# Kernel optimization log

Hardware: AMD Instinct MI355X
Metric: run time of the kernel (lower is better)

Reference implementation:

```python
import jax, jax.numpy as jnp
import numpy as np

N_NODES = 50_000
N_EDGES = 1_600_000
D = 128          # input_dim == hidden_dim
L = 3            # num_layers
NUM_GRAPHS = 64
LN_EPS = 1e-5


def setup_inputs() -> dict:
    key = jax.random.key(0)
    ks = jax.random.split(key, 12)
    x = jax.random.normal(ks[0], (N_NODES, D), dtype=jnp.float32)
    edge_index = jax.random.randint(ks[1], (2, N_EDGES), 0, N_NODES, dtype=jnp.int64)
    edge_weight = jax.random.normal(ks[2], (N_EDGES,), dtype=jnp.float32)  # signed
    batch = jnp.sort(jax.random.randint(ks[3], (N_NODES,), 0, NUM_GRAPHS, dtype=jnp.int64))
    W_pos = jax.random.normal(ks[4], (L, D, D), dtype=jnp.float32) * 0.05
    b_pos = jnp.zeros((L, D), dtype=jnp.float32)
    W_neg = jax.random.normal(ks[5], (L, D, D), dtype=jnp.float32) * 0.05
    b_neg = jnp.zeros((L, D), dtype=jnp.float32)
    ln_gamma = jnp.ones((D,), dtype=jnp.float32)
    ln_beta = jnp.zeros((D,), dtype=jnp.float32)
    return dict(x=x, edge_index=edge_index, edge_weight=edge_weight, batch=batch,
                W_pos=W_pos, b_pos=b_pos, W_neg=W_neg, b_neg=b_neg,
                ln_gamma=ln_gamma, ln_beta=ln_beta)


def gcn_conv(x, src, dst, w, W, b):
    """PyG GCNConv with edge weights: lin -> sym-normalized scatter-add -> +bias.
    Self-loops (weight 1) are handled analytically instead of appending edges.
    Edges with weight 0 contribute nothing (equivalent to sign-masking the edge set)."""
    n = x.shape[0]
    xw = x @ W                                              # [N, D]
    deg = jax.ops.segment_sum(w, dst, num_segments=n) + 1.0  # +1 for self-loop; >= 1
    dinv = jax.lax.rsqrt(deg)                                # deg^{-1/2}
    norm = dinv[src] * w * dinv[dst]                         # [E]
    agg = jax.ops.segment_sum(norm[:, None] * xw[src], dst, num_segments=n)
    agg = agg + (dinv * dinv)[:, None] * xw                  # self-loop message: xw / deg
    return agg + b


def reference(x, edge_index, edge_weight, batch, W_pos, b_pos, W_neg, b_neg, ln_gamma, ln_beta):
    src, dst = edge_index[0], edge_index[1]
    # sign-split as zero-weight edges: identical math to boolean-masked edge subsets
    w_pos = jnp.maximum(edge_weight, 0.0)
    w_neg = jnp.maximum(-edge_weight, 0.0)
    for l in range(L):
        px = gcn_conv(x, src, dst, w_pos, W_pos[l], b_pos[l])
        nx = gcn_conv(x, src, dst, w_neg, W_neg[l], b_neg[l])
        x = jax.nn.relu(px) - jax.nn.relu(nx)
    # global_mean_pool
    sums = jax.ops.segment_sum(x, batch, num_segments=NUM_GRAPHS)
    counts = jax.ops.segment_sum(jnp.ones((x.shape[0],), x.dtype), batch, num_segments=NUM_GRAPHS)
    pooled = sums / jnp.maximum(counts, 1.0)[:, None]        # [G, D]
    # LayerNorm over feature dim
    mu = pooled.mean(-1, keepdims=True)
    var = ((pooled - mu) ** 2).mean(-1, keepdims=True)
    return (pooled - mu) * jax.lax.rsqrt(var + LN_EPS) * ln_gamma + ln_beta
```

## Files before the change

### kernel.cpp

```cpp
#include <hip/hip_runtime.h>
#include <hip/hip_fp16.h>

#define D 128
#define NG 64
#define WPB 4
#define TILE 4096
#define BSH 7
#define BNODES 128
#define CAP 4608
#define MASK40 ((1ULL << 40) - 1)
#define FPSCALE 1048576.0f
#define INV_FPSCALE (1.0f / 1048576.0f)
#define GEMM_GRID 512
typedef unsigned int uint;
typedef unsigned long long u64;
typedef _Float16 f16x8 __attribute__((ext_vector_type(8)));
typedef float f32x4 __attribute__((ext_vector_type(4)));

__global__ void k_prep(const float* __restrict__ x, __half* __restrict__ xo,
                       const float* __restrict__ Wp, const float* __restrict__ Wn,
                       __half* __restrict__ wpt, __half* __restrict__ wnt,
                       float* sums, float* cnt, int* bktcur,
                       int total4, int nbuk) {
    int i = blockIdx.x * blockDim.x + threadIdx.x;
    if (i < total4) {
        float4 f = ((const float4*)x)[i];
        __half2 h0 = __floats2half2_rn(f.x, f.y);
        __half2 h1 = __floats2half2_rn(f.z, f.w);
        uint2 st;
        st.x = *(uint*)&h0; st.y = *(uint*)&h1;
        ((uint2*)xo)[i] = st;
    }
    if (i < 3 * 128 * 128) {
        int l = i >> 14;
        int r = i & 16383;
        int col = r >> 7, k = r & 127;
        size_t src = ((size_t)l << 14) + ((size_t)k << 7) + col;
        wpt[i] = __float2half_rn(Wp[src]);
        wnt[i] = __float2half_rn(Wn[src]);
    }
    if (i < NG * D) sums[i] = 0.0f;
    if (i < NG) cnt[i] = 0.0f;
    if (i < nbuk) bktcur[i] = i * CAP;
}

__global__ __launch_bounds__(256) void k_bucket(const int* __restrict__ ei,
                                                const float* __restrict__ ew,
                                                int* bktcur, uint2* rec,
                                                int E, int nbuk) {
    __shared__ int h2[256];
    __shared__ int lofs[512];
    __shared__ int gbase[512];
    __shared__ int lcur[512];
    __shared__ uint2 stg[TILE];
    int t = threadIdx.x;
    lofs[t] = 0; lofs[t + 256] = 0;
    __syncthreads();
    int lo = blockIdx.x * TILE, hi = min(E, lo + TILE);
    int m = hi - lo;
    for (int e = lo + t; e < hi; e += 256)
        atomicAdd(&lofs[ei[(size_t)E + e] >> BSH], 1);
    __syncthreads();
    int c0 = lofs[2 * t], c1 = lofs[2 * t + 1];
    if (c0) gbase[2 * t] = atomicAdd(&bktcur[2 * t], c0);
    if (c1) gbase[2 * t + 1] = atomicAdd(&bktcur[2 * t + 1], c1);
    h2[t] = c0 + c1;
    __syncthreads();
    for (int off = 1; off < 256; off <<= 1) {
        int u = (t >= off) ? h2[t - off] : 0;
        __syncthreads();
        h2[t] += u;
        __syncthreads();
    }
    int excl = h2[t] - (c0 + c1);
    lofs[2 * t] = excl;
    lofs[2 * t + 1] = excl + c0;
    lcur[2 * t] = excl;
    lcur[2 * t + 1] = excl + c0;
    __syncthreads();
    for (int e = lo + t; e < hi; e += 256) {
        int dst = ei[(size_t)E + e];
        int src = ei[e];
        float w = ew[e];
        int b = dst >> BSH;
        int pos = atomicAdd(&lcur[b], 1);
        stg[pos] = make_uint2((uint)src | ((uint)(dst & (BNODES - 1)) << 16) |
                                  ((uint)b << 23),
                              __float_as_uint(w));
    }
    __syncthreads();
    for (int i = t; i < m; i += 256) {
        uint2 r = stg[i];
        int b = (int)(r.x >> 23);
        int gpos = gbase[b] + (i - lofs[b]);
        if (gpos < (b + 1) * CAP)
            rec[gpos] = r;
    }
}

__global__ __launch_bounds__(256) void k_deg(const uint2* __restrict__ rec,
                                             const int* __restrict__ bktcur,
                                             float2* dpn, int* row_ptr,
                                             int* cend, int* cpos, int n) {
    __shared__ u64 accp[BNODES], accn[BNODES];
    __shared__ int s[BNODES];
    int b = blockIdx.x, t = threadIdx.x;
    if (t < BNODES) { accp[t] = 0ULL; accn[t] = 0ULL; }
    __syncthreads();
    int lo = b * CAP, hi = bktcur[b];
    for (int i = lo + t; i < hi; i += 256) {
        uint2 r = rec[i];
        int dl = (r.x >> 16) & (BNODES - 1);
        float w = __uint_as_float(r.y);
        u64 pkt = (1ULL << 40) | (u64)(fabsf(w) * FPSCALE + 0.5f);
        atomicAdd((w < 0.0f) ? &accn[dl] : &accp[dl], pkt);
    }
    __syncthreads();
    int cp = 0, cn = 0, cnt_t = 0;
    u64 p = 0, q = 0;
    if (t < BNODES) {
        p = accp[t]; q = accn[t];
        cp = (int)(p >> 40); cn = (int)(q >> 40);
        cnt_t = cp + cn;
        s[t] = cnt_t;
    }
    __syncthreads();
    for (int off = 1; off < BNODES; off <<= 1) {
        int u = 0;
        if (t < BNODES && t >= off) u = s[t - off];
        __syncthreads();
        if (t < BNODES) s[t] += u;
        __syncthreads();
    }
    if (t < BNODES) {
        int node = b * BNODES + t;
        if (node < n) {
            int base = b * CAP + s[t] - cnt_t;
            row_ptr[node] = base;
            cend[node] = base + cnt_t;
            cpos[node] = cp;
            float2 dd;
            dd.x = rsqrtf(1.0f + (float)(p & MASK40) * INV_FPSCALE);
            dd.y = rsqrtf(1.0f + (float)(q & MASK40) * INV_FPSCALE);
            dpn[node] = dd;
        }
    }
}

__global__ __launch_bounds__(256) void k_csr(const uint2* __restrict__ rec,
                                             const int* __restrict__ bktcur,
                                             const int* __restrict__ row_ptr,
                                             const int* __restrict__ cpos,
                                             const float2* __restrict__ dpn,
                                             uint* pack, int n) {
    __shared__ int curp[BNODES], curn[BNODES];
    int b = blockIdx.x, t = threadIdx.x;
    if (t < BNODES) {
        int node = b * BNODES + t;
        if (node < n) {
            int rp = row_ptr[node];
            curp[t] = rp;
            curn[t] = rp + cpos[node];
        } else { curp[t] = 0; curn[t] = 0; }
    }
    __syncthreads();
    int lo = b * CAP, hi = bktcur[b];
    for (int i = lo + t; i < hi; i += 256) {
        uint2 r = rec[i];
        int src = r.x & 0xFFFFu;
        int dl = (r.x >> 16) & (BNODES - 1);
        float w = __uint_as_float(r.y);
        float2 dd = dpn[src];
        float v;
        int slot;
        if (w < 0.0f) { v = dd.y * (-w); slot = atomicAdd(&curn[dl], 1); }
        else          { v = dd.x * w;    slot = atomicAdd(&curp[dl], 1); }
        pack[slot] = (uint)src | ((uint)__half_as_ushort(__float2half_rn(v)) << 16);
    }
}

__global__ __launch_bounds__(64 * WPB) void k_gather(
    const __half* __restrict__ x16, const uint* __restrict__ pack,
    const int* __restrict__ row_ptr, const int* __restrict__ cend,
    const int* __restrict__ cpos, const float2* __restrict__ dpn,
    __half* __restrict__ tp, __half* __restrict__ tn, int n) {
    __shared__ uint eb[WPB][136];
    const int w = threadIdx.x >> 6;
    const int lane = threadIdx.x & 63;
    const int q = lane >> 4;
    const int c = lane & 15;
    const int node = blockIdx.x * WPB + w;
    if (node >= n) return;
    const int beg = row_ptr[node], end = cend[node];
    const int mid = beg + cpos[node];
    const float2 dd = dpn[node];
    const uint4* __restrict__ x4u = (const uint4*)x16;
    uint* ebw = eb[w];

    uint4 xv = x4u[(size_t)node * 16 + c];
    float xf[8];
    {
        float2 f;
        f = __half22float2(*(__half2*)&xv.x); xf[0] = f.x; xf[1] = f.y;
        f = __half22float2(*(__half2*)&xv.y); xf[2] = f.x; xf[3] = f.y;
        f = __half22float2(*(__half2*)&xv.z); xf[4] = f.x; xf[5] = f.y;
        f = __half22float2(*(__half2*)&xv.w); xf[6] = f.x; xf[7] = f.y;
    }

#pragma unroll
    for (int part = 0; part < 2; ++part) {
        const int lo = part ? mid : beg;
        const int hi = part ? end : mid;
        const float ds = part ? dd.y : dd.x;
        float a0[8], a1[8];
        const float s0 = (q == 0) ? ds : 0.0f;
#pragma unroll
        for (int j = 0; j < 8; ++j) { a0[j] = s0 * xf[j]; a1[j] = 0.0f; }
        for (int cb = lo; cb < hi; cb += 128) {
            int m = hi - cb;
            if (m > 128) m = 128;
            const int mp = (m + 7) & ~7;
            for (int i = lane; i < mp; i += 64)
                ebw[i] = (i < m) ? pack[cb + i] : 0u;
            for (int i = 0; i < mp; i += 8) {
                const uint pk0 = ebw[i + q];
                const uint pk1 = ebw[i + 4 + q];
                const uint4 y0 = x4u[(size_t)(pk0 & 0xFFFFu) * 16 + c];
                const uint4 y1 = x4u[(size_t)(pk1 & 0xFFFFu) * 16 + c];
                const float v0 =
                    __half2float(__ushort_as_half((unsigned short)(pk0 >> 16)));
                const float v1 =
                    __half2float(__ushort_as_half((unsigned short)(pk1 >> 16)));
                float2 f;
                f = __half22float2(*(__half2*)&y0.x);
                a0[0] = fmaf(v0, f.x, a0[0]); a0[1] = fmaf(v0, f.y, a0[1]);
                f = __half22float2(*(__half2*)&y0.y);
                a0[2] = fmaf(v0, f.x, a0[2]); a0[3] = fmaf(v0, f.y, a0[3]);
                f = __half22float2(*(__half2*)&y0.z);
                a0[4] = fmaf(v0, f.x, a0[4]); a0[5] = fmaf(v0, f.y, a0[5]);
                f = __half22float2(*(__half2*)&y0.w);
                a0[6] = fmaf(v0, f.x, a0[6]); a0[7] = fmaf(v0, f.y, a0[7]);
                f = __half22float2(*(__half2*)&y1.x);
                a1[0] = fmaf(v1, f.x, a1[0]); a1[1] = fmaf(v1, f.y, a1[1]);
                f = __half22float2(*(__half2*)&y1.y);
                a1[2] = fmaf(v1, f.x, a1[2]); a1[3] = fmaf(v1, f.y, a1[3]);
                f = __half22float2(*(__half2*)&y1.z);
                a1[4] = fmaf(v1, f.x, a1[4]); a1[5] = fmaf(v1, f.y, a1[5]);
                f = __half22float2(*(__half2*)&y1.w);
                a1[6] = fmaf(v1, f.x, a1[6]); a1[7] = fmaf(v1, f.y, a1[7]);
            }
        }
#pragma unroll
        for (int j = 0; j < 8; ++j) {
            a0[j] += a1[j];
            a0[j] += __shfl_down(a0[j], 32);
            a0[j] += __shfl_down(a0[j], 16);
        }
        if (q == 0) {
            __half2 h0 = __floats2half2_rn(ds * a0[0], ds * a0[1]);
            __half2 h1 = __floats2half2_rn(ds * a0[2], ds * a0[3]);
            __half2 h2 = __floats2half2_rn(ds * a0[4], ds * a0[5]);
            __half2 h3 = __floats2half2_rn(ds * a0[6], ds * a0[7]);
            uint4 st;
            st.x = *(uint*)&h0; st.y = *(uint*)&h1;
            st.z = *(uint*)&h2; st.w = *(uint*)&h3;
            ((uint4*)(part ? tn : tp))[(size_t)node * 16 + c] = st;
        }
    }
}

__global__ __launch_bounds__(256) void k_gemm(
    const __half* __restrict__ tp, const __half* __restrict__ tn,
    const __half* __restrict__ wpt, const __half* __restrict__ wnt,
    const float* __restrict__ bp, const float* __restrict__ bn,
    __half* __restrict__ xout, int nrows, int ntiles) {
    __shared__ __half wlds[2][128][136];
    const int tid = threadIdx.x;
    {
        const uint4* wp4 = (const uint4*)wpt;
        const uint4* wn4 = (const uint4*)wnt;
#pragma unroll
        for (int j = 0; j < 8; ++j) {
            int idx = tid + j * 256;
            int col = idx >> 4;
            int k8 = idx & 15;
            *(uint4*)&wlds[0][col][k8 * 8] = wp4[idx];
            *(uint4*)&wlds[1][col][k8 * 8] = wn4[idx];
        }
    }
    const int wave = tid >> 6;
    const int lane = tid & 63;
    const int cl = lane & 15;
    const int quad = lane >> 4;
    __syncthreads();
    for (int rt = blockIdx.x; rt < ntiles; rt += GEMM_GRID) {
        const int row_blk = rt * 64 + wave * 16;
        if (row_blk >= nrows) continue;
        int arow = row_blk + cl;
        if (arow >= nrows) arow = nrows - 1;
        const f16x8* __restrict__ tpr = (const f16x8*)(tp + (size_t)arow * 128);
        const f16x8* __restrict__ tnr = (const f16x8*)(tn + (size_t)arow * 128);
        f16x8 ap[4], an[4];
#pragma unroll
        for (int kb = 0; kb < 4; ++kb) {
            ap[kb] = tpr[kb * 4 + quad];
            an[kb] = tnr[kb * 4 + quad];
        }
#pragma unroll
        for (int ct = 0; ct < 8; ++ct) {
            const int col = ct * 16 + cl;
            f32x4 accp = {0.0f, 0.0f, 0.0f, 0.0f};
            f32x4 accn = {0.0f, 0.0f, 0.0f, 0.0f};
#pragma unroll
            for (int kb = 0; kb < 4; ++kb) {
                f16x8 wfp = *(const f16x8*)&wlds[0][col][kb * 32 + quad * 8];
                f16x8 wfn = *(const f16x8*)&wlds[1][col][kb * 32 + quad * 8];
                accp = __builtin_amdgcn_mfma_f32_16x16x32_f16(ap[kb], wfp, accp,
                                                              0, 0, 0);
                accn = __builtin_amdgcn_mfma_f32_16x16x32_f16(an[kb], wfn, accn,
                                                              0, 0, 0);
            }
            const float bpv = bp[col], bnv = bn[col];
#pragma unroll
            for (int reg = 0; reg < 4; ++reg) {
                int row = row_blk + quad * 4 + reg;
                if (row < nrows) {
                    float pv = accp[reg] + bpv;
                    float nv = accn[reg] + bnv;
                    xout[(size_t)row * 128 + col] =
                        __float2half_rn(fmaxf(pv, 0.0f) - fmaxf(nv, 0.0f));
                }
            }
        }
    }
}

__global__ __launch_bounds__(128) void k_pool(
    const __half* __restrict__ x, const int* __restrict__ batch,
    float* sums, float* cnt, int n) {
    int f = threadIdx.x;
    int n0 = blockIdx.x * 64;
    int n1 = min(n0 + 64, n);
    float acc = 0.0f;
    int g_prev = batch[n0];
    int local = 0;
    for (int i = n0; i < n1; ++i) {
        int g = batch[i];
        if (g != g_prev) {
            atomicAdd(&sums[g_prev * D + f], acc);
            if (f == 0) atomicAdd(&cnt[g_prev], (float)local);
            acc = 0.0f; local = 0; g_prev = g;
        }
        acc += __half2float(x[(size_t)i * D + f]);
        local++;
    }
    atomicAdd(&sums[g_prev * D + f], acc);
    if (f == 0) atomicAdd(&cnt[g_prev], (float)local);
}

__global__ __launch_bounds__(128) void k_ln(
    const float* __restrict__ sums, const float* __restrict__ cnt,
    const float* __restrict__ gamma, const float* __restrict__ beta,
    float* __restrict__ out) {
    __shared__ float red[128];
    int g = blockIdx.x, f = threadIdx.x;
    float c = fmaxf(cnt[g], 1.0f);
    float v = sums[g * D + f] / c;
    red[f] = v;
    __syncthreads();
    for (int off = 64; off > 0; off >>= 1) {
        if (f < off) red[f] += red[f + off];
        __syncthreads();
    }
    float mu = red[0] / (float)D;
    __syncthreads();
    float d = v - mu;
    red[f] = d * d;
    __syncthreads();
    for (int off = 64; off > 0; off >>= 1) {
        if (f < off) red[f] += red[f + off];
        __syncthreads();
    }
    float var = red[0] / (float)D;
    out[g * D + f] = d * rsqrtf(var + 1e-5f) * gamma[f] + beta[f];
}

extern "C" void kernel_launch(void* const* d_in, const int* in_sizes, int n_in,
                              void* d_out, int out_size, void* d_ws,
                              size_t ws_size, hipStream_t stream) {
    const float* x     = (const float*)d_in[0];
    const int*   ei    = (const int*)d_in[1];
    const float* ew    = (const float*)d_in[2];
    const int*   bat   = (const int*)d_in[3];
    const float* Wp    = (const float*)d_in[4];
    const float* bp    = (const float*)d_in[5];
    const float* Wn    = (const float*)d_in[6];
    const float* bn    = (const float*)d_in[7];
    const float* gamma = (const float*)d_in[8];
    const float* beta  = (const float*)d_in[9];
    const int n = in_sizes[0] / D;
    const int E = in_sizes[2];
    const int NBUK = (n + BNODES - 1) >> BSH;
    const int NBLK = (E + TILE - 1) / TILE;
    const int NT = (n + 63) / 64;

    float* ws = (float*)d_ws;
    size_t off = 0;
    auto alloc = [&](size_t elems) {
        float* p = ws + off;
        off += (elems + 63) & ~(size_t)63;
        return p;
    };
    __half* x16  = (__half*)alloc((size_t)n * D / 2);
    __half* tpb  = (__half*)alloc((size_t)n * D / 2);
    __half* tnb  = (__half*)alloc((size_t)n * D / 2);
    __half* xb   = (__half*)alloc((size_t)n * D / 2);
    __half* wpt  = (__half*)alloc(3 * 128 * 128 / 2);
    __half* wnt  = (__half*)alloc(3 * 128 * 128 / 2);
    float2* dpn  = (float2*)alloc((size_t)2 * n);
    float* sums  = alloc(NG * D);
    float* cnt   = alloc(NG);
    int* bktcur  = (int*)alloc(NBUK);
    int* row_ptr = (int*)alloc(n);
    int* cend    = (int*)alloc(n);
    int* cpos    = (int*)alloc(n);
    uint2* rec   = (uint2*)alloc((size_t)NBUK * CAP * 2);
    uint* pack   = (uint*)alloc((size_t)NBUK * CAP);

    k_prep<<<(n * D / 4 + 255) / 256, 256, 0, stream>>>(
        x, x16, Wp, Wn, wpt, wnt, sums, cnt, bktcur, n * D / 4, NBUK);
    k_bucket<<<NBLK, 256, 0, stream>>>(ei, ew, bktcur, rec, E, NBUK);
    k_deg<<<NBUK, 256, 0, stream>>>(rec, bktcur, dpn, row_ptr, cend, cpos, n);
    k_csr<<<NBUK, 256, 0, stream>>>(rec, bktcur, row_ptr, cpos, dpn, pack, n);

    const __half* xcur = x16;
    for (int l = 0; l < 3; ++l) {
        k_gather<<<(n + WPB - 1) / WPB, 64 * WPB, 0, stream>>>(
            xcur, pack, row_ptr, cend, cpos, dpn, tpb, tnb, n);
        k_gemm<<<GEMM_GRID, 256, 0, stream>>>(
            tpb, tnb, wpt + (size_t)l * 128 * 128, wnt + (size_t)l * 128 * 128,
            bp + (size_t)l * D, bn + (size_t)l * D, xb, n, NT);
        xcur = xb;
    }
    k_pool<<<(n + 63) / 64, 128, 0, stream>>>(xb, bat, sums, cnt, n);
    k_ln<<<NG, 128, 0, stream>>>(sums, cnt, gamma, beta, (float*)d_out);
}
```

Before: 385.8 us.

## Fuse graph-build kernels cooperatively, widen gather unroll, merge pool and layernorm

Merges the prep, bucket, degree and CSR kernels into one cooperative kernel with grid-wide syncs between phases, which removes several launch boundaries. It also widens the gather inner loop to four independent edge loads and accumulators per step for more memory-level parallelism. Pooling and LayerNorm become one kernel that binary-searches each graph's node range in the sorted batch array, so the global atomics and the zeroing of sums and counts are no longer needed. The risks are the cooperative launch: the grid (max of tile and bucket counts, about 391 blocks) must be co-resident, and 32KB+ of shared memory per block limits occupancy. The pooling now runs on only 64 blocks, which may leave the GPU underused.

New measurement: 614.5 us. +59.3%, slower.

```diff
diff --git a/kernel.cpp b/kernel.cpp
--- a/kernel.cpp
+++ b/kernel.cpp
@@ -1,5 +1,8 @@
 #include <hip/hip_runtime.h>
 #include <hip/hip_fp16.h>
+#include <hip/hip_cooperative_groups.h>
+
+namespace cg = cooperative_groups;
 
 #define D 128
 #define NG 64
@@ -17,21 +20,29 @@
 typedef _Float16 f16x8 __attribute__((ext_vector_type(8)));
 typedef float f32x4 __attribute__((ext_vector_type(4)));
 
-__global__ void k_prep(const float* __restrict__ x, __half* __restrict__ xo,
-                       const float* __restrict__ Wp, const float* __restrict__ Wn,
-                       __half* __restrict__ wpt, __half* __restrict__ wnt,
-                       float* sums, float* cnt, int* bktcur,
-                       int total4, int nbuk) {
-    int i = blockIdx.x * blockDim.x + threadIdx.x;
-    if (i < total4) {
+__global__ __launch_bounds__(256) void k_build(
+    const float* __restrict__ x, const int* __restrict__ ei,
+    const float* __restrict__ ew, __half* __restrict__ x16,
+    const float* __restrict__ Wp, const float* __restrict__ Wn,
+    __half* __restrict__ wpt, __half* __restrict__ wnt,
+    int* bktcur, uint2* rec, float2* dpn, int* row_ptr, int* cend, int* cpos,
+    uint* pack, int n, int E, int nbuk, int nblk, int total4) {
+    cg::grid_group grid = cg::this_grid();
+    __shared__ uint2 stg[TILE];
+    __shared__ int meta[1792];
+    const int t = threadIdx.x;
+    const int gtid = blockIdx.x * 256 + t;
+    const int gstride = gridDim.x * 256;
+
+    for (int i = gtid; i < total4; i += gstride) {
         float4 f = ((const float4*)x)[i];
         __half2 h0 = __floats2half2_rn(f.x, f.y);
         __half2 h1 = __floats2half2_rn(f.z, f.w);
         uint2 st;
         st.x = *(uint*)&h0; st.y = *(uint*)&h1;
-        ((uint2*)xo)[i] = st;
-    }
-    if (i < 3 * 128 * 128) {
+        ((uint2*)x16)[i] = st;
+    }
+    for (int i = gtid; i < 3 * 128 * 128; i += gstride) {
         int l = i >> 14;
         int r = i & 16383;
         int col = r >> 7, k = r & 127;
@@ -39,143 +50,142 @@
         wpt[i] = __float2half_rn(Wp[src]);
         wnt[i] = __float2half_rn(Wn[src]);
     }
-    if (i < NG * D) sums[i] = 0.0f;
-    if (i < NG) cnt[i] = 0.0f;
-    if (i < nbuk) bktcur[i] = i * CAP;
-}
-
-__global__ __launch_bounds__(256) void k_bucket(const int* __restrict__ ei,
-                                                const float* __restrict__ ew,
-                                                int* bktcur, uint2* rec,
-                                                int E, int nbuk) {
-    __shared__ int h2[256];
-    __shared__ int lofs[512];
-    __shared__ int gbase[512];
-    __shared__ int lcur[512];
-    __shared__ uint2 stg[TILE];
-    int t = threadIdx.x;
-    lofs[t] = 0; lofs[t + 256] = 0;
-    __syncthreads();
-    int lo = blockIdx.x * TILE, hi = min(E, lo + TILE);
-    int m = hi - lo;
-    for (int e = lo + t; e < hi; e += 256)
-        atomicAdd(&lofs[ei[(size_t)E + e] >> BSH], 1);
-    __syncthreads();
-    int c0 = lofs[2 * t], c1 = lofs[2 * t + 1];
-    if (c0) gbase[2 * t] = atomicAdd(&bktcur[2 * t], c0);
-    if (c1) gbase[2 * t + 1] = atomicAdd(&bktcur[2 * t + 1], c1);
-    h2[t] = c0 + c1;
-    __syncthreads();
-    for (int off = 1; off < 256; off <<= 1) {
-        int u = (t >= off) ? h2[t - off] : 0;
-        __syncthreads();
-        h2[t] += u;
-        __syncthreads();
-    }
-    int excl = h2[t] - (c0 + c1);
-    lofs[2 * t] = excl;
-    lofs[2 * t + 1] = excl + c0;
-    lcur[2 * t] = excl;
-    lcur[2 * t + 1] = excl + c0;
-    __syncthreads();
-    for (int e = lo + t; e < hi; e += 256) {
-        int dst = ei[(size_t)E + e];
-        int src = ei[e];
-        float w = ew[e];
-        int b = dst >> BSH;
-        int pos = atomicAdd(&lcur[b], 1);
-        stg[pos] = make_uint2((uint)src | ((uint)(dst & (BNODES - 1)) << 16) |
-                                  ((uint)b << 23),
-                              __float_as_uint(w));
-    }
-    __syncthreads();
-    for (int i = t; i < m; i += 256) {
-        uint2 r = stg[i];
-        int b = (int)(r.x >> 23);
-        int gpos = gbase[b] + (i - lofs[b]);
-        if (gpos < (b + 1) * CAP)
-            rec[gpos] = r;
-    }
-}
-
-__global__ __launch_bounds__(256) void k_deg(const uint2* __restrict__ rec,
-                                             const int* __restrict__ bktcur,
-                                             float2* dpn, int* row_ptr,
-                                             int* cend, int* cpos, int n) {
-    __shared__ u64 accp[BNODES], accn[BNODES];
-    __shared__ int s[BNODES];
-    int b = blockIdx.x, t = threadIdx.x;
-    if (t < BNODES) { accp[t] = 0ULL; accn[t] = 0ULL; }
-    __syncthreads();
-    int lo = b * CAP, hi = bktcur[b];
-    for (int i = lo + t; i < hi; i += 256) {
-        uint2 r = rec[i];
-        int dl = (r.x >> 16) & (BNODES - 1);
-        float w = __uint_as_float(r.y);
-        u64 pkt = (1ULL << 40) | (u64)(fabsf(w) * FPSCALE + 0.5f);
-        atomicAdd((w < 0.0f) ? &accn[dl] : &accp[dl], pkt);
-    }
-    __syncthreads();
-    int cp = 0, cn = 0, cnt_t = 0;
-    u64 p = 0, q = 0;
-    if (t < BNODES) {
-        p = accp[t]; q = accn[t];
-        cp = (int)(p >> 40); cn = (int)(q >> 40);
-        cnt_t = cp + cn;
-        s[t] = cnt_t;
-    }
-    __syncthreads();
-    for (int off = 1; off < BNODES; off <<= 1) {
-        int u = 0;
-        if (t < BNODES && t >= off) u = s[t - off];
-        __syncthreads();
-        if (t < BNODES) s[t] += u;
-        __syncthreads();
-    }
-    if (t < BNODES) {
-        int node = b * BNODES + t;
-        if (node < n) {
-            int base = b * CAP + s[t] - cnt_t;
-            row_ptr[node] = base;
-            cend[node] = base + cnt_t;
-            cpos[node] = cp;
-            float2 dd;
-            dd.x = rsqrtf(1.0f + (float)(p & MASK40) * INV_FPSCALE);
-            dd.y = rsqrtf(1.0f + (float)(q & MASK40) * INV_FPSCALE);
-            dpn[node] = dd;
-        }
-    }
-}
-
-__global__ __launch_bounds__(256) void k_csr(const uint2* __restrict__ rec,
-                                             const int* __restrict__ bktcur,
-                                             const int* __restrict__ row_ptr,
-                                             const int* __restrict__ cpos,
-                                             const float2* __restrict__ dpn,
-                                             uint* pack, int n) {
-    __shared__ int curp[BNODES], curn[BNODES];
-    int b = blockIdx.x, t = threadIdx.x;
-    if (t < BNODES) {
-        int node = b * BNODES + t;
-        if (node < n) {
-            int rp = row_ptr[node];
-            curp[t] = rp;
-            curn[t] = rp + cpos[node];
-        } else { curp[t] = 0; curn[t] = 0; }
-    }
-    __syncthreads();
-    int lo = b * CAP, hi = bktcur[b];
-    for (int i = lo + t; i < hi; i += 256) {
-        uint2 r = rec[i];
-        int src = r.x & 0xFFFFu;
-        int dl = (r.x >> 16) & (BNODES - 1);
-        float w = __uint_as_float(r.y);
-        float2 dd = dpn[src];
-        float v;
-        int slot;
-        if (w < 0.0f) { v = dd.y * (-w); slot = atomicAdd(&curn[dl], 1); }
-        else          { v = dd.x * w;    slot = atomicAdd(&curp[dl], 1); }
-        pack[slot] = (uint)src | ((uint)__half_as_ushort(__float2half_rn(v)) << 16);
+    for (int i = gtid; i < nbuk; i += gstride) bktcur[i] = i * CAP;
+    grid.sync();
+
+    {
+        int* h2 = meta;
+        int* lofs = meta + 256;
+        int* gbase = meta + 768;
+        int* lcur = meta + 1280;
+        for (int blk = blockIdx.x; blk < nblk; blk += gridDim.x) {
+            lofs[t] = 0; lofs[t + 256] = 0;
+            __syncthreads();
+            int lo = blk * TILE, hi = min(E, lo + TILE);
+            int m = hi - lo;
+            for (int e = lo + t; e < hi; e += 256)
+                atomicAdd(&lofs[ei[(size_t)E + e] >> BSH], 1);
+            __syncthreads();
+            int c0 = lofs[2 * t], c1 = lofs[2 * t + 1];
+            if (c0) gbase[2 * t] = atomicAdd(&bktcur[2 * t], c0);
+            if (c1) gbase[2 * t + 1] = atomicAdd(&bktcur[2 * t + 1], c1);
+            h2[t] = c0 + c1;
+            __syncthreads();
+            for (int off = 1; off < 256; off <<= 1) {
+                int u = (t >= off) ? h2[t - off] : 0;
+                __syncthreads();
+                h2[t] += u;
+                __syncthreads();
+            }
+            int excl = h2[t] - (c0 + c1);
+            lofs[2 * t] = excl;
+            lofs[2 * t + 1] = excl + c0;
+            lcur[2 * t] = excl;
+            lcur[2 * t + 1] = excl + c0;
+            __syncthreads();
+            for (int e = lo + t; e < hi; e += 256) {
+                int dst = ei[(size_t)E + e];
+                int src = ei[e];
+                float w = ew[e];
+                int b = dst >> BSH;
+                int pos = atomicAdd(&lcur[b], 1);
+                stg[pos] = make_uint2((uint)src |
+                                          ((uint)(dst & (BNODES - 1)) << 16) |
+                                          ((uint)b << 23),
+                                      __float_as_uint(w));
+            }
+            __syncthreads();
+            for (int i = t; i < m; i += 256) {
+                uint2 r = stg[i];
+                int b = (int)(r.x >> 23);
+                int gpos = gbase[b] + (i - lofs[b]);
+                if (gpos < (b + 1) * CAP)
+                    rec[gpos] = r;
+            }
+            __syncthreads();
+        }
+    }
+    grid.sync();
+
+    {
+        u64* accp = (u64*)stg;
+        u64* accn = accp + BNODES;
+        int* s = meta;
+        for (int b = blockIdx.x; b < nbuk; b += gridDim.x) {
+            if (t < BNODES) { accp[t] = 0ULL; accn[t] = 0ULL; }
+            __syncthreads();
+            int lo = b * CAP, hi = bktcur[b];
+            for (int i = lo + t; i < hi; i += 256) {
+                uint2 r = rec[i];
+                int dl = (r.x >> 16) & (BNODES - 1);
+                float w = __uint_as_float(r.y);
+                u64 pkt = (1ULL << 40) | (u64)(fabsf(w) * FPSCALE + 0.5f);
+                atomicAdd((w < 0.0f) ? &accn[dl] : &accp[dl], pkt);
+            }
+            __syncthreads();
+            int cp = 0, cn = 0, cnt_t = 0;
+            u64 p = 0, q = 0;
+            if (t < BNODES) {
+                p = accp[t]; q = accn[t];
+                cp = (int)(p >> 40); cn = (int)(q >> 40);
+                cnt_t = cp + cn;
+                s[t] = cnt_t;
+            }
+            __syncthreads();
+            for (int off = 1; off < BNODES; off <<= 1) {
+                int u = 0;
+                if (t < BNODES && t >= off) u = s[t - off];
+                __syncthreads();
+                if (t < BNODES) s[t] += u;
+                __syncthreads();
+            }
+            if (t < BNODES) {
+                int node = b * BNODES + t;
+                if (node < n) {
+                    int base = b * CAP + s[t] - cnt_t;
+                    row_ptr[node] = base;
+                    cend[node] = base + cnt_t;
+                    cpos[node] = cp;
+                    float2 dd;
+                    dd.x = rsqrtf(1.0f + (float)(p & MASK40) * INV_FPSCALE);
+                    dd.y = rsqrtf(1.0f + (float)(q & MASK40) * INV_FPSCALE);
+                    dpn[node] = dd;
+                }
+            }
+            __syncthreads();
+        }
+    }
+    grid.sync();
+
+    {
+        int* curp = meta;
+        int* curn = meta + BNODES;
+        for (int b = blockIdx.x; b < nbuk; b += gridDim.x) {
+            if (t < BNODES) {
+                int node = b * BNODES + t;
+                if (node < n) {
+                    int rp = row_ptr[node];
+                    curp[t] = rp;
+                    curn[t] = rp + cpos[node];
+                } else { curp[t] = 0; curn[t] = 0; }
+            }
+            __syncthreads();
+            int lo = b * CAP, hi = bktcur[b];
+            for (int i = lo + t; i < hi; i += 256) {
+                uint2 r = rec[i];
+                int src = r.x & 0xFFFFu;
+                int dl = (r.x >> 16) & (BNODES - 1);
+                float w = __uint_as_float(r.y);
+                float2 dd = dpn[src];
+                float v;
+                int slot;
+                if (w < 0.0f) { v = dd.y * (-w); slot = atomicAdd(&curn[dl], 1); }
+                else          { v = dd.x * w;    slot = atomicAdd(&curp[dl], 1); }
+                pack[slot] =
+                    (uint)src | ((uint)__half_as_ushort(__float2half_rn(v)) << 16);
+            }
+            __syncthreads();
+        }
     }
 }
 
@@ -212,25 +222,35 @@
         const int lo = part ? mid : beg;
         const int hi = part ? end : mid;
         const float ds = part ? dd.y : dd.x;
-        float a0[8], a1[8];
+        float a0[8], a1[8], a2[8], a3[8];
         const float s0 = (q == 0) ? ds : 0.0f;
 #pragma unroll
-        for (int j = 0; j < 8; ++j) { a0[j] = s0 * xf[j]; a1[j] = 0.0f; }
+        for (int j = 0; j < 8; ++j) {
+            a0[j] = s0 * xf[j]; a1[j] = 0.0f; a2[j] = 0.0f; a3[j] = 0.0f;
+        }
         for (int cb = lo; cb < hi; cb += 128) {
             int m = hi - cb;
             if (m > 128) m = 128;
-            const int mp = (m + 7) & ~7;
+            const int mp = (m + 15) & ~15;
             for (int i = lane; i < mp; i += 64)
                 ebw[i] = (i < m) ? pack[cb + i] : 0u;
-            for (int i = 0; i < mp; i += 8) {
+            for (int i = 0; i < mp; i += 16) {
                 const uint pk0 = ebw[i + q];
                 const uint pk1 = ebw[i + 4 + q];
+                const uint pk2 = ebw[i + 8 + q];
+                const uint pk3 = ebw[i + 12 + q];
                 const uint4 y0 = x4u[(size_t)(pk0 & 0xFFFFu) * 16 + c];
                 const uint4 y1 = x4u[(size_t)(pk1 & 0xFFFFu) * 16 + c];
+                const uint4 y2 = x4u[(size_t)(pk2 & 0xFFFFu) * 16 + c];
+                const uint4 y3 = x4u[(size_t)(pk3 & 0xFFFFu) * 16 + c];
                 const float v0 =
                     __half2float(__ushort_as_half((unsigned short)(pk0 >> 16)));
                 const float v1 =
                     __half2float(__ushort_as_half((unsigned short)(pk1 >> 16)));
+                const float v2 =
+                    __half2float(__ushort_as_half((unsigned short)(pk2 >> 16)));
+                const float v3 =
+                    __half2float(__ushort_as_half((unsigned short)(pk3 >> 16)));
                 float2 f;
                 f = __half22float2(*(__half2*)&y0.x);
                 a0[0] = fmaf(v0, f.x, a0[0]); a0[1] = fmaf(v0, f.y, a0[1]);
@@ -248,11 +268,27 @@
                 a1[4] = fmaf(v1, f.x, a1[4]); a1[5] = fmaf(v1, f.y, a1[5]);
                 f = __half22float2(*(__half2*)&y1.w);
                 a1[6] = fmaf(v1, f.x, a1[6]); a1[7] = fmaf(v1, f.y, a1[7]);
+                f = __half22float2(*(__half2*)&y2.x);
+                a2[0] = fmaf(v2, f.x, a2[0]); a2[1] = fmaf(v2, f.y, a2[1]);
+                f = __half22float2(*(__half2*)&y2.y);
+                a2[2] = fmaf(v2, f.x, a2[2]); a2[3] = fmaf(v2, f.y, a2[3]);
+                f = __half22float2(*(__half2*)&y2.z);
+                a2[4] = fmaf(v2, f.x, a2[4]); a2[5] = fmaf(v2, f.y, a2[5]);
+                f = __half22float2(*(__half2*)&y2.w);
+                a2[6] = fmaf(v2, f.x, a2[6]); a2[7] = fmaf(v2, f.y, a2[7]);
+                f = __half22float2(*(__half2*)&y3.x);
+                a3[0] = fmaf(v3, f.x, a3[0]); a3[1] = fmaf(v3, f.y, a3[1]);
+                f = __half22float2(*(__half2*)&y3.y);
+                a3[2] = fmaf(v3, f.x, a3[2]); a3[3] = fmaf(v3, f.y, a3[3]);
+                f = __half22float2(*(__half2*)&y3.z);
+                a3[4] = fmaf(v3, f.x, a3[4]); a3[5] = fmaf(v3, f.y, a3[5]);
+                f = __half22float2(*(__half2*)&y3.w);
+                a3[6] = fmaf(v3, f.x, a3[6]); a3[7] = fmaf(v3, f.y, a3[7]);
             }
         }
 #pragma unroll
         for (int j = 0; j < 8; ++j) {
-            a0[j] += a1[j];
+            a0[j] += a1[j] + a2[j] + a3[j];
             a0[j] += __shfl_down(a0[j], 32);
             a0[j] += __shfl_down(a0[j], 16);
         }
@@ -335,37 +371,29 @@
     }
 }
 
-__global__ __launch_bounds__(128) void k_pool(
+__global__ __launch_bounds__(128) void k_poolln(
     const __half* __restrict__ x, const int* __restrict__ batch,
-    float* sums, float* cnt, int n) {
-    int f = threadIdx.x;
-    int n0 = blockIdx.x * 64;
-    int n1 = min(n0 + 64, n);
-    float acc = 0.0f;
-    int g_prev = batch[n0];
-    int local = 0;
-    for (int i = n0; i < n1; ++i) {
-        int g = batch[i];
-        if (g != g_prev) {
-            atomicAdd(&sums[g_prev * D + f], acc);
-            if (f == 0) atomicAdd(&cnt[g_prev], (float)local);
-            acc = 0.0f; local = 0; g_prev = g;
-        }
-        acc += __half2float(x[(size_t)i * D + f]);
-        local++;
-    }
-    atomicAdd(&sums[g_prev * D + f], acc);
-    if (f == 0) atomicAdd(&cnt[g_prev], (float)local);
-}
-
-__global__ __launch_bounds__(128) void k_ln(
-    const float* __restrict__ sums, const float* __restrict__ cnt,
     const float* __restrict__ gamma, const float* __restrict__ beta,
-    float* __restrict__ out) {
+    float* __restrict__ out, int n) {
     __shared__ float red[128];
     int g = blockIdx.x, f = threadIdx.x;
-    float c = fmaxf(cnt[g], 1.0f);
-    float v = sums[g * D + f] / c;
+    int lo = 0, hi = n;
+    while (lo < hi) { int mid = (lo + hi) >> 1; if (batch[mid] < g) lo = mid + 1; else hi = mid; }
+    int r0 = lo;
+    lo = r0; hi = n;
+    while (lo < hi) { int mid = (lo + hi) >> 1; if (batch[mid] < g + 1) lo = mid + 1; else hi = mid; }
+    int r1 = lo;
+    float acc0 = 0.0f, acc1 = 0.0f, acc2 = 0.0f, acc3 = 0.0f;
+    int i = r0;
+    for (; i + 3 < r1; i += 4) {
+        acc0 += __half2float(x[(size_t)i * D + f]);
+        acc1 += __half2float(x[(size_t)(i + 1) * D + f]);
+        acc2 += __half2float(x[(size_t)(i + 2) * D + f]);
+        acc3 += __half2float(x[(size_t)(i + 3) * D + f]);
+    }
+    for (; i < r1; ++i) acc0 += __half2float(x[(size_t)i * D + f]);
+    float cntf = (float)(r1 - r0);
+    float v = (acc0 + acc1 + acc2 + acc3) / fmaxf(cntf, 1.0f);
     red[f] = v;
     __syncthreads();
     for (int off = 64; off > 0; off >>= 1) {
@@ -398,11 +426,13 @@
     const float* bn    = (const float*)d_in[7];
     const float* gamma = (const float*)d_in[8];
     const float* beta  = (const float*)d_in[9];
-    const int n = in_sizes[0] / D;
-    const int E = in_sizes[2];
-    const int NBUK = (n + BNODES - 1) >> BSH;
-    const int NBLK = (E + TILE - 1) / TILE;
+    int n = in_sizes[0] / D;
+    int E = in_sizes[2];
+    int NBUK = (n + BNODES - 1) >> BSH;
+    int NBLK = (E + TILE - 1) / TILE;
     const int NT = (n + 63) / 64;
+    int total4 = n * D / 4;
+    const int GRID = (NBLK > NBUK) ? NBLK : NBUK;
 
     float* ws = (float*)d_ws;
     size_t off = 0;
@@ -418,8 +448,6 @@
     __half* wpt  = (__half*)alloc(3 * 128 * 128 / 2);
     __half* wnt  = (__half*)alloc(3 * 128 * 128 / 2);
     float2* dpn  = (float2*)alloc((size_t)2 * n);
-    float* sums  = alloc(NG * D);
-    float* cnt   = alloc(NG);
     int* bktcur  = (int*)alloc(NBUK);
     int* row_ptr = (int*)alloc(n);
     int* cend    = (int*)alloc(n);
@@ -427,11 +455,15 @@
     uint2* rec   = (uint2*)alloc((size_t)NBUK * CAP * 2);
     uint* pack   = (uint*)alloc((size_t)NBUK * CAP);
 
-    k_prep<<<(n * D / 4 + 255) / 256, 256, 0, stream>>>(
-        x, x16, Wp, Wn, wpt, wnt, sums, cnt, bktcur, n * D / 4, NBUK);
-    k_bucket<<<NBLK, 256, 0, stream>>>(ei, ew, bktcur, rec, E, NBUK);
-    k_deg<<<NBUK, 256, 0, stream>>>(rec, bktcur, dpn, row_ptr, cend, cpos, n);
-    k_csr<<<NBUK, 256, 0, stream>>>(rec, bktcur, row_ptr, cpos, dpn, pack, n);
+    void* kargs[] = {(void*)&x,       (void*)&ei,     (void*)&ew,
+                     (void*)&x16,     (void*)&Wp,     (void*)&Wn,
+                     (void*)&wpt,     (void*)&wnt,    (void*)&bktcur,
+                     (void*)&rec,     (void*)&dpn,    (void*)&row_ptr,
+                     (void*)&cend,    (void*)&cpos,   (void*)&pack,
+                     (void*)&n,       (void*)&E,      (void*)&NBUK,
+                     (void*)&NBLK,    (void*)&total4};
+    hipLaunchCooperativeKernel((const void*)k_build, dim3(GRID), dim3(256),
+                               kargs, 0, stream);
 
     const __half* xcur = x16;
     for (int l = 0; l < 3; ++l) {
@@ -442,6 +474,5 @@
             bp + (size_t)l * D, bn + (size_t)l * D, xb, n, NT);
         xcur = xb;
     }
-    k_pool<<<(n + 63) / 64, 128, 0, stream>>>(xb, bat, sums, cnt, n);
-    k_ln<<<NG, 128, 0, stream>>>(sums, cnt, gamma, beta, (float*)d_out);
+    k_poolln<<<NG, 128, 0, stream>>>(xb, bat, gamma, beta, (float*)d_out, n);
 }
```
